# Kernel tuning notes

Hardware: AMD Instinct MI355X
Metric: run time of the kernel (lower is better)

The kernel has to match this reference:

```python
import jax, jax.numpy as jnp
import numpy as np

BATCH = 2048
VOCAB = 50257
TOPK = 512


def setup_inputs() -> dict:
    key = jax.random.key(0)
    k1, k2 = jax.random.split(key)
    features = jax.random.normal(k1, (BATCH, VOCAB), dtype=jnp.float32)
    labels = jax.random.randint(k2, (BATCH,), 0, VOCAB, dtype=jnp.int64 if jax.config.jax_enable_x64 else jnp.int32)
    return {"features": features, "labels": labels, "k": TOPK}


def reference(features, labels, k):
    # features: [B, V], labels: [B], k: python int (top-k count)
    # Original per-sample loop computes: -log(exp(feat_label) / sum(exp(topk(row))))
    # Vectorized: mean over batch of (log(sum(exp(topk_vals))) - feat_label).
    feat_label = jnp.take_along_axis(features, labels[:, None].astype(jnp.int32), axis=1)[:, 0]  # [B]
    topk_vals, _ = jax.lax.top_k(features, k)  # [B, k]
    lse = jnp.log(jnp.sum(jnp.exp(topk_vals), axis=-1))  # [B] (matches original non-stabilized math)
    return jnp.mean(lse - feat_label)
```

## Files before the change

kernel.cpp:

```cpp
#include <hip/hip_runtime.h>
#include <cstdint>
#include <cstddef>

#define BATCH 2048
#define VOCAB 50257
#define TOPK  512
#define CAND_MAX 4096
#define BLOCK 256

typedef float vfloat4 __attribute__((ext_vector_type(4)));

__device__ __forceinline__ unsigned fkey(float f) {
    unsigned u = __float_as_uint(f);
    return (u & 0x80000000u) ? ~u : (u | 0x80000000u);
}
__device__ __forceinline__ float unfkey(unsigned k) {
    unsigned u = (k & 0x80000000u) ? (k & 0x7FFFFFFFu) : ~k;
    return __uint_as_float(u);
}

__global__ __launch_bounds__(BLOCK) void topk_ce_kernel(
    const float* __restrict__ feats,
    const int*   __restrict__ labels,
    float*       __restrict__ out)
{
    __shared__ float    cand[CAND_MAX];
    __shared__ int      s_cnt;
    __shared__ unsigned s_hist[256];
    __shared__ unsigned s_sfx[256];
    __shared__ int      s_dig, s_above;
    __shared__ float    s_psum[BLOCK / 64];
    __shared__ float    s_pcnt[BLOCK / 64];

    const int row = blockIdx.x;
    const int tid = threadIdx.x;
    const float* rp = feats + (size_t)row * VOCAB;

    uintptr_t a = (uintptr_t)rp;
    int head = ((int)((16u - (a & 15u)) & 15u)) >> 2;
    if (head > VOCAB) head = VOCAB;
    const int nvec = (VOCAB - head) >> 2;
    const int tailstart = head + nvec * 4;
    const vfloat4* vp = (const vfloat4*)(rp + head);
    const int nfull = nvec / (BLOCK * 4);
    const int restart = nfull * BLOCK * 4;

    float thresh = 2.0f;
    float blo = 0.0f, bhi = 0.0f;
    bool  has_lo = false, has_hi = false;
    float step = 1.0f;
    int   n_cand = 0;

#define APPEND1(x) do { if ((x) > thresh) { int p_ = atomicAdd(&s_cnt, 1); \
                        if (p_ < CAND_MAX) cand[p_] = (x); } } while (0)
#define APPEND4(v) do { APPEND1((v).x); APPEND1((v).y); APPEND1((v).z); APPEND1((v).w); } while (0)

    for (int attempt = 0; attempt < 40; ++attempt) {
        if (tid == 0) s_cnt = 0;
        __syncthreads();

        for (int i = tid; i < head; i += BLOCK) {
            float v = rp[i];
            APPEND1(v);
        }
        for (int it = 0; it < nfull; ++it) {
            const int base = it * (BLOCK * 4) + tid;
            vfloat4 v0 = __builtin_nontemporal_load(&vp[base]);
            vfloat4 v1 = __builtin_nontemporal_load(&vp[base + BLOCK]);
            vfloat4 v2 = __builtin_nontemporal_load(&vp[base + 2 * BLOCK]);
            vfloat4 v3 = __builtin_nontemporal_load(&vp[base + 3 * BLOCK]);
            APPEND4(v0); APPEND4(v1); APPEND4(v2); APPEND4(v3);
        }
        for (int i = restart + tid; i < nvec; i += BLOCK) {
            vfloat4 v = __builtin_nontemporal_load(&vp[i]);
            APPEND4(v);
        }
        for (int i = tailstart + tid; i < VOCAB; i += BLOCK) {
            float v = rp[i];
            APPEND1(v);
        }
        __syncthreads();
        n_cand = s_cnt;
        if (n_cand >= TOPK && n_cand <= CAND_MAX) break;
        if (n_cand < TOPK) { bhi = thresh; has_hi = true; }
        else               { blo = thresh; has_lo = true; }
        if (has_lo && has_hi)      thresh = 0.5f * (blo + bhi);
        else if (has_lo)          { thresh = blo + step; step *= 2.0f; }
        else                      { thresh = bhi - step; step *= 2.0f; }
        __syncthreads();
    }

    const int m  = (n_cand < CAND_MAX) ? n_cand : CAND_MAX;
    const int kk = (TOPK < m) ? TOPK : m;
    if (m == 0) return;

    unsigned pref = 0, maskhi = 0;
    int remain = kk;
    const int m_pad = ((m + BLOCK - 1) / BLOCK) * BLOCK;

    for (int sh = 24; sh >= 0; sh -= 8) {
        s_hist[tid] = 0;
        __syncthreads();

        for (int i = tid; i < m_pad; i += BLOCK) {
            bool valid = (i < m);
            unsigned key = valid ? fkey(cand[i]) : 0u;
            bool match = valid && ((key & maskhi) == pref);
            unsigned dig = (key >> sh) & 255u;
            unsigned long long mm = __ballot(match);
            if (mm) {
                int leader = __ffsll((unsigned long long)mm) - 1;
                unsigned ldig = __shfl(dig, leader);
                unsigned long long same = __ballot(match && (dig == ldig));
                if (same == mm) {
                    if ((tid & 63) == leader)
                        atomicAdd(&s_hist[ldig], (unsigned)__popcll(mm));
                } else if (match) {
                    atomicAdd(&s_hist[dig], 1u);
                }
            }
        }
        __syncthreads();

        s_sfx[tid] = s_hist[tid];
        __syncthreads();
        for (int off = 1; off < 256; off <<= 1) {
            unsigned add = (tid + off < 256) ? s_sfx[tid + off] : 0u;
            __syncthreads();
            s_sfx[tid] += add;
            __syncthreads();
        }
        unsigned my  = s_sfx[tid];
        unsigned nxt = (tid < 255) ? s_sfx[tid + 1] : 0u;
        if ((int)my >= remain && (tid == 255 || (int)nxt < remain)) {
            s_dig = tid;
            s_above = (int)nxt;
        }
        __syncthreads();
        remain -= s_above;
        pref   |= ((unsigned)s_dig) << sh;
        maskhi |= (0xFFu << sh);
        __syncthreads();
    }

    const float tval = unfkey(pref);

    float psum = 0.0f, pcnt = 0.0f;
    for (int i = tid; i < m; i += BLOCK) {
        float v = cand[i];
        if (fkey(v) > pref) { psum += expf(v); pcnt += 1.0f; }
    }
    for (int off = 32; off > 0; off >>= 1) {
        psum += __shfl_down(psum, off);
        pcnt += __shfl_down(pcnt, off);
    }
    const int lane = tid & 63, wid = tid >> 6;
    if (lane == 0) { s_psum[wid] = psum; s_pcnt[wid] = pcnt; }
    __syncthreads();
    if (tid == 0) {
        float sum = 0.0f, cnt = 0.0f;
        for (int w = 0; w < BLOCK / 64; ++w) { sum += s_psum[w]; cnt += s_pcnt[w]; }
        sum += ((float)kk - cnt) * expf(tval);
        float fl = rp[labels[row]];
        float loss = logf(sum) - fl;
        atomicAdd(out, loss * (1.0f / (float)BATCH));
    }
}

extern "C" void kernel_launch(void* const* d_in, const int* in_sizes, int n_in,
                              void* d_out, int out_size, void* d_ws, size_t ws_size,
                              hipStream_t stream) {
    const float* feats  = (const float*)d_in[0];
    const int*   labels = (const int*)d_in[1];
    float* out = (float*)d_out;
    (void)in_sizes; (void)n_in; (void)out_size; (void)d_ws; (void)ws_size;

    (void)hipMemsetAsync(out, 0, sizeof(float), stream);
    topk_ce_kernel<<<BATCH, BLOCK, 0, stream>>>(feats, labels, out);
}
```

Measured before the change: 527.4 us.

## Replace shared atomic candidate append with per-wave ballot compaction and segments

Candidate collection now uses wave-level ballot and mbcnt prefix counts to write into a per-wave segment of shared memory, instead of one shared atomic counter per element. The main streaming loop also software-pipelines its vector loads one iteration ahead. The suffix scan over the histogram is changed from a barrier-heavy shared-memory scan to wave shuffles plus a small cross-wave combine. The aim is to remove LDS atomic contention and barriers. In exchange, per-wave segment overflow can force extra threshold passes, and the prefetch raises register use.

```diff
diff --git a/kernel.cpp b/kernel.cpp
--- a/kernel.cpp
+++ b/kernel.cpp
@@ -7,6 +7,8 @@
 #define TOPK  512
 #define CAND_MAX 4096
 #define BLOCK 256
+#define NWAVE (BLOCK / 64)
+#define WSEG  (CAND_MAX / NWAVE)
 
 typedef float vfloat4 __attribute__((ext_vector_type(4)));
 
@@ -25,15 +27,18 @@
     float*       __restrict__ out)
 {
     __shared__ float    cand[CAND_MAX];
-    __shared__ int      s_cnt;
+    __shared__ int      s_wc[NWAVE];
     __shared__ unsigned s_hist[256];
     __shared__ unsigned s_sfx[256];
+    __shared__ unsigned s_wtot[NWAVE];
     __shared__ int      s_dig, s_above;
-    __shared__ float    s_psum[BLOCK / 64];
-    __shared__ float    s_pcnt[BLOCK / 64];
-
-    const int row = blockIdx.x;
-    const int tid = threadIdx.x;
+    __shared__ float    s_psum[NWAVE];
+    __shared__ float    s_pcnt[NWAVE];
+
+    const int row  = blockIdx.x;
+    const int tid  = threadIdx.x;
+    const int lane = tid & 63;
+    const int wid  = tid >> 6;
     const float* rp = feats + (size_t)row * VOCAB;
 
     uintptr_t a = (uintptr_t)rp;
@@ -45,67 +50,109 @@
     const int nfull = nvec / (BLOCK * 4);
     const int restart = nfull * BLOCK * 4;
 
+    const float NEGINF = -__builtin_inff();
+
     float thresh = 2.0f;
     float blo = 0.0f, bhi = 0.0f;
     bool  has_lo = false, has_hi = false;
     float step = 1.0f;
-    int   n_cand = 0;
-
-#define APPEND1(x) do { if ((x) > thresh) { int p_ = atomicAdd(&s_cnt, 1); \
-                        if (p_ < CAND_MAX) cand[p_] = (x); } } while (0)
+
+#define APPEND1(x) do { \
+        bool p_ = (x) > thresh; \
+        unsigned long long m_ = __ballot(p_); \
+        if (m_) { \
+            int pre_ = __builtin_amdgcn_mbcnt_hi((unsigned)(m_ >> 32), \
+                         __builtin_amdgcn_mbcnt_lo((unsigned)m_, 0u)); \
+            int pos_ = wbase + pre_; \
+            if (p_ && pos_ < wlimit) cand[pos_] = (x); \
+            wbase += (int)__popcll(m_); \
+        } } while (0)
 #define APPEND4(v) do { APPEND1((v).x); APPEND1((v).y); APPEND1((v).z); APPEND1((v).w); } while (0)
 
     for (int attempt = 0; attempt < 40; ++attempt) {
-        if (tid == 0) s_cnt = 0;
-        __syncthreads();
-
-        for (int i = tid; i < head; i += BLOCK) {
-            float v = rp[i];
+        int wbase = wid * WSEG;
+        const int wstart = wbase;
+        const int wlimit = wstart + WSEG;
+
+        for (int i0 = 0; i0 < head; i0 += BLOCK) {
+            int i = i0 + tid;
+            float v = NEGINF;
+            if (i < head) v = rp[i];
             APPEND1(v);
         }
-        for (int it = 0; it < nfull; ++it) {
-            const int base = it * (BLOCK * 4) + tid;
-            vfloat4 v0 = __builtin_nontemporal_load(&vp[base]);
-            vfloat4 v1 = __builtin_nontemporal_load(&vp[base + BLOCK]);
-            vfloat4 v2 = __builtin_nontemporal_load(&vp[base + 2 * BLOCK]);
-            vfloat4 v3 = __builtin_nontemporal_load(&vp[base + 3 * BLOCK]);
-            APPEND4(v0); APPEND4(v1); APPEND4(v2); APPEND4(v3);
-        }
-        for (int i = restart + tid; i < nvec; i += BLOCK) {
-            vfloat4 v = __builtin_nontemporal_load(&vp[i]);
+
+        if (nfull > 0) {
+            vfloat4 n0 = __builtin_nontemporal_load(&vp[tid]);
+            vfloat4 n1 = __builtin_nontemporal_load(&vp[tid + BLOCK]);
+            vfloat4 n2 = __builtin_nontemporal_load(&vp[tid + 2 * BLOCK]);
+            vfloat4 n3 = __builtin_nontemporal_load(&vp[tid + 3 * BLOCK]);
+            for (int it = 0; it < nfull; ++it) {
+                vfloat4 c0 = n0, c1 = n1, c2 = n2, c3 = n3;
+                if (it + 1 < nfull) {
+                    const int bn = (it + 1) * (BLOCK * 4) + tid;
+                    n0 = __builtin_nontemporal_load(&vp[bn]);
+                    n1 = __builtin_nontemporal_load(&vp[bn + BLOCK]);
+                    n2 = __builtin_nontemporal_load(&vp[bn + 2 * BLOCK]);
+                    n3 = __builtin_nontemporal_load(&vp[bn + 3 * BLOCK]);
+                }
+                APPEND4(c0); APPEND4(c1); APPEND4(c2); APPEND4(c3);
+            }
+        }
+
+        for (int i0 = restart; i0 < nvec; i0 += BLOCK) {
+            int i = i0 + tid;
+            vfloat4 v = { NEGINF, NEGINF, NEGINF, NEGINF };
+            if (i < nvec) v = __builtin_nontemporal_load(&vp[i]);
             APPEND4(v);
         }
-        for (int i = tailstart + tid; i < VOCAB; i += BLOCK) {
-            float v = rp[i];
+        for (int i0 = tailstart; i0 < VOCAB; i0 += BLOCK) {
+            int i = i0 + tid;
+            float v = NEGINF;
+            if (i < VOCAB) v = rp[i];
             APPEND1(v);
         }
-        __syncthreads();
-        n_cand = s_cnt;
-        if (n_cand >= TOPK && n_cand <= CAND_MAX) break;
-        if (n_cand < TOPK) { bhi = thresh; has_hi = true; }
-        else               { blo = thresh; has_lo = true; }
+
+        if (lane == 0) s_wc[wid] = wbase - wstart;
+        __syncthreads();
+        int total = 0, wmax = 0;
+#pragma unroll
+        for (int w = 0; w < NWAVE; ++w) {
+            int c = s_wc[w];
+            total += c;
+            if (c > wmax) wmax = c;
+        }
+        if (total >= TOPK && total <= CAND_MAX && wmax <= WSEG) break;
+        if (total < TOPK) { bhi = thresh; has_hi = true; }
+        else              { blo = thresh; has_lo = true; }
         if (has_lo && has_hi)      thresh = 0.5f * (blo + bhi);
         else if (has_lo)          { thresh = blo + step; step *= 2.0f; }
         else                      { thresh = bhi - step; step *= 2.0f; }
         __syncthreads();
     }
-
-    const int m  = (n_cand < CAND_MAX) ? n_cand : CAND_MAX;
-    const int kk = (TOPK < m) ? TOPK : m;
-    if (m == 0) return;
+#undef APPEND1
+#undef APPEND4
+
+    int wc_mine = s_wc[wid]; if (wc_mine > WSEG) wc_mine = WSEG;
+    int m_stored = 0;
+#pragma unroll
+    for (int w = 0; w < NWAVE; ++w) {
+        int c = s_wc[w];
+        m_stored += (c > WSEG) ? WSEG : c;
+    }
+    if (m_stored == 0) return;
+    const int kk = (TOPK < m_stored) ? TOPK : m_stored;
+    const int segbase = wid * WSEG;
 
     unsigned pref = 0, maskhi = 0;
     int remain = kk;
-    const int m_pad = ((m + BLOCK - 1) / BLOCK) * BLOCK;
 
     for (int sh = 24; sh >= 0; sh -= 8) {
         s_hist[tid] = 0;
         __syncthreads();
 
-        for (int i = tid; i < m_pad; i += BLOCK) {
-            bool valid = (i < m);
-            unsigned key = valid ? fkey(cand[i]) : 0u;
-            bool match = valid && ((key & maskhi) == pref);
+        for (int i = lane; i < wc_mine; i += 64) {
+            unsigned key = fkey(cand[segbase + i]);
+            bool match = ((key & maskhi) == pref);
             unsigned dig = (key >> sh) & 255u;
             unsigned long long mm = __ballot(match);
             if (mm) {
@@ -113,7 +160,7 @@
                 unsigned ldig = __shfl(dig, leader);
                 unsigned long long same = __ballot(match && (dig == ldig));
                 if (same == mm) {
-                    if ((tid & 63) == leader)
+                    if (lane == leader)
                         atomicAdd(&s_hist[ldig], (unsigned)__popcll(mm));
                 } else if (match) {
                     atomicAdd(&s_hist[dig], 1u);
@@ -122,15 +169,21 @@
         }
         __syncthreads();
 
-        s_sfx[tid] = s_hist[tid];
-        __syncthreads();
-        for (int off = 1; off < 256; off <<= 1) {
-            unsigned add = (tid + off < 256) ? s_sfx[tid + off] : 0u;
-            __syncthreads();
-            s_sfx[tid] += add;
-            __syncthreads();
-        }
-        unsigned my  = s_sfx[tid];
+        unsigned v = s_hist[tid];
+#pragma unroll
+        for (int off = 1; off < 64; off <<= 1) {
+            unsigned o = __shfl_down(v, off);
+            if (lane + off < 64) v += o;
+        }
+        if (lane == 0) s_wtot[wid] = v;
+        __syncthreads();
+        unsigned addv = 0;
+#pragma unroll
+        for (int w = 0; w < NWAVE; ++w)
+            if (w > wid) addv += s_wtot[w];
+        unsigned my = v + addv;
+        s_sfx[tid] = my;
+        __syncthreads();
         unsigned nxt = (tid < 255) ? s_sfx[tid + 1] : 0u;
         if ((int)my >= remain && (tid == 255 || (int)nxt < remain)) {
             s_dig = tid;
@@ -146,20 +199,20 @@
     const float tval = unfkey(pref);
 
     float psum = 0.0f, pcnt = 0.0f;
-    for (int i = tid; i < m; i += BLOCK) {
-        float v = cand[i];
+    for (int i = lane; i < wc_mine; i += 64) {
+        float v = cand[segbase + i];
         if (fkey(v) > pref) { psum += expf(v); pcnt += 1.0f; }
     }
+#pragma unroll
     for (int off = 32; off > 0; off >>= 1) {
         psum += __shfl_down(psum, off);
         pcnt += __shfl_down(pcnt, off);
     }
-    const int lane = tid & 63, wid = tid >> 6;
     if (lane == 0) { s_psum[wid] = psum; s_pcnt[wid] = pcnt; }
     __syncthreads();
     if (tid == 0) {
         float sum = 0.0f, cnt = 0.0f;
-        for (int w = 0; w < BLOCK / 64; ++w) { sum += s_psum[w]; cnt += s_pcnt[w]; }
+        for (int w = 0; w < NWAVE; ++w) { sum += s_psum[w]; cnt += s_pcnt[w]; }
         sum += ((float)kk - cnt) * expf(tval);
         float fl = rp[labels[row]];
         float loss = logf(sum) - fl;
```

After: 513.9 us. 2.6% less time.
